# Kernel tuning notes

Hardware: AMD Instinct MI355X
Metric: run time of the kernel (lower is better)

## Reference

```python
import jax, jax.numpy as jnp
import numpy as np

PAD = (1, 1, 1, 1)  # (left, right, top, bottom)
STRIDE = 1

def _blur_kernel(dtype):
    k = jnp.asarray([1.0, 3.0, 3.0, 1.0], dtype=dtype)
    k2 = k[:, None] * k[None, :]
    k2 = k2 / k2.sum()  # normalize=True -> divide by 64
    return k2

def setup_inputs() -> dict:
    key = jax.random.key(0)
    x = jax.random.normal(key, (8, 64, 512, 512), dtype=jnp.float32)
    return {"x": x}

def reference(x):
    B, C, H, W = x.shape
    k2 = _blur_kernel(x.dtype)
    # depthwise kernel: OIHW with O=C, I=1 and feature_group_count=C
    kernel = jnp.broadcast_to(k2[None, None], (C, 1, 4, 4))
    # F.pad order: (left, right, top, bottom) -> pad W then H
    xp = jnp.pad(x, ((0, 0), (0, 0), (PAD[2], PAD[3]), (PAD[0], PAD[1])))
    out = jax.lax.conv_general_dilated(
        xp, kernel,
        window_strides=(STRIDE, STRIDE),
        padding='VALID',
        dimension_numbers=('NCHW', 'OIHW', 'NCHW'),
        feature_group_count=C,
    )
    return out
```

## Files before the change

### kernel.cpp

```cpp
#include <hip/hip_runtime.h>


constexpr int H  = 512;
constexpr int W  = 512;
constexpr int OH = 511;
constexpr int OW = 511;
constexpr int NPLANES = 8 * 64;

typedef float f4u __attribute__((ext_vector_type(4), aligned(4)));

struct Row { float4 A, B, C; };

__device__ __forceinline__ Row ldrow(const float* __restrict__ ip, int gy,
                                     int cb, bool aok, bool cok)
{
    Row r;
    r.A = make_float4(0.f, 0.f, 0.f, 0.f);
    r.B = r.A;
    r.C = r.A;
    if ((unsigned)gy < (unsigned)H) {
        const float* p = ip + (size_t)gy * W + cb;
        r.B = *reinterpret_cast<const float4*>(p);
        if (aok) r.A = *reinterpret_cast<const float4*>(p - 4);
        if (cok) r.C = *reinterpret_cast<const float4*>(p + 4);
    }
    return r;
}

__device__ __forceinline__ float4 hp(const Row& r)
{
    float4 h;
    h.x = (r.A.w + r.B.z) + 3.f * (r.B.x + r.B.y);
    h.y = (r.B.x + r.B.w) + 3.f * (r.B.y + r.B.z);
    h.z = (r.B.y + r.C.x) + 3.f * (r.B.z + r.B.w);
    h.w = (r.B.z + r.C.y) + 3.f * (r.B.w + r.C.x);
    return h;
}

__device__ __forceinline__ float4 vcomb(const float4& h0, const float4& h1,
                                        const float4& h2, const float4& h3)
{
    float4 o;
    o.x = ((h0.x + h3.x) + 3.f * (h1.x + h2.x)) * 0.015625f;
    o.y = ((h0.y + h3.y) + 3.f * (h1.y + h2.y)) * 0.015625f;
    o.z = ((h0.z + h3.z) + 3.f * (h1.z + h2.z)) * 0.015625f;
    o.w = ((h0.w + h3.w) + 3.f * (h1.w + h2.w)) * 0.015625f;
    return o;
}

__device__ __forceinline__ void st(float* __restrict__ op, int oy, int cb,
                                   bool cok, const float4& o)
{
    float* p = op + (size_t)oy * OW + cb;
    if (cok) {
        *reinterpret_cast<f4u*>(p) = (f4u){o.x, o.y, o.z, o.w};
    } else {
        p[0] = o.x; p[1] = o.y; p[2] = o.z;
    }
}

__global__ __launch_bounds__(256)
void blur_kernel(const float* __restrict__ in, float* __restrict__ out)
{
    const int tid   = threadIdx.x;
    const int xt    = tid & 127;
    const int sub   = tid >> 7;
    const int cb    = xt * 4;
    const int plane = blockIdx.x;
    const int ys    = blockIdx.y * 128 + sub * 64;
    const int ye    = min(ys + 64, OH);

    const float* __restrict__ ip = in  + (size_t)plane * (H * W);
    float*       __restrict__ op = out + (size_t)plane * (OH * OW);

    const bool aok = (xt > 0);
    const bool cok = (xt < 127);

    Row r0 = ldrow(ip, ys - 1, cb, aok, cok);
    Row r1 = ldrow(ip, ys,     cb, aok, cok);
    Row r2 = ldrow(ip, ys + 1, cb, aok, cok);
    Row P  = ldrow(ip, ys + 2, cb, aok, cok);
    Row Q  = ldrow(ip, ys + 3, cb, aok, cok);

    float4 h0 = hp(r0);
    float4 h1 = hp(r1);
    float4 h2 = hp(r2);

    int oy = ys;
    while (oy + 1 < ye) {
        float4 h3 = hp(P);
        st(op, oy, cb, cok, vcomb(h0, h1, h2, h3));
        P = ldrow(ip, oy + 4, cb, aok, cok);

        float4 h4 = hp(Q);
        st(op, oy + 1, cb, cok, vcomb(h1, h2, h3, h4));
        Q = ldrow(ip, oy + 5, cb, aok, cok);

        h0 = h2; h1 = h3; h2 = h4;
        oy += 2;
    }
    if (oy < ye) {
        float4 h3 = hp(P);
        st(op, oy, cb, cok, vcomb(h0, h1, h2, h3));
    }
}

extern "C" void kernel_launch(void* const* d_in, const int* in_sizes, int n_in,
                              void* d_out, int out_size, void* d_ws, size_t ws_size,
                              hipStream_t stream)
{
    const float* x = (const float*)d_in[0];
    float* out = (float*)d_out;

    dim3 grid(NPLANES, 4);
    dim3 block(256);
    blur_kernel<<<grid, block, 0, stream>>>(x, out);
}
```

Baseline: 270.4 us.

## Use 8 columns per lane with wavefront shuffles for horizontal halo

Each lane now covers 8 columns, so one 64-lane wavefront spans a full 512-wide row. The horizontal halo comes from neighbouring lanes via shuffles instead of extra overlapping float4 loads. Each wave handles 32 rows with four rows of prefetch in flight, and the last lane's edge column is handled with an overlapping store. This removes redundant global loads and the per-thread halo branches, at the cost of more registers per thread and fewer threads per plane row.

```diff
diff --git a/kernel.cpp b/kernel.cpp
--- a/kernel.cpp
+++ b/kernel.cpp
@@ -9,99 +9,98 @@
 
 typedef float f4u __attribute__((ext_vector_type(4), aligned(4)));
 
-struct Row { float4 A, B, C; };
+struct H8 { float v[8]; };
+struct R2 { float4 b0, b1; };
 
-__device__ __forceinline__ Row ldrow(const float* __restrict__ ip, int gy,
-                                     int cb, bool aok, bool cok)
+__device__ __forceinline__ R2 ldrow(const float* __restrict__ ip, int gy, int cb)
 {
-    Row r;
-    r.A = make_float4(0.f, 0.f, 0.f, 0.f);
-    r.B = r.A;
-    r.C = r.A;
+    R2 r;
+    r.b0 = make_float4(0.f, 0.f, 0.f, 0.f);
+    r.b1 = r.b0;
     if ((unsigned)gy < (unsigned)H) {
         const float* p = ip + (size_t)gy * W + cb;
-        r.B = *reinterpret_cast<const float4*>(p);
-        if (aok) r.A = *reinterpret_cast<const float4*>(p - 4);
-        if (cok) r.C = *reinterpret_cast<const float4*>(p + 4);
+        r.b0 = *reinterpret_cast<const float4*>(p);
+        r.b1 = *reinterpret_cast<const float4*>(p + 4);
     }
     return r;
 }
 
-__device__ __forceinline__ float4 hp(const Row& r)
+__device__ __forceinline__ H8 hp8(const R2& r, bool l0, bool l63)
 {
-    float4 h;
-    h.x = (r.A.w + r.B.z) + 3.f * (r.B.x + r.B.y);
-    h.y = (r.B.x + r.B.w) + 3.f * (r.B.y + r.B.z);
-    h.z = (r.B.y + r.C.x) + 3.f * (r.B.z + r.B.w);
-    h.w = (r.B.z + r.C.y) + 3.f * (r.B.w + r.C.x);
+    float L  = __shfl_up(r.b1.w, 1);
+    float RX = __shfl_down(r.b0.x, 1);
+    float RY = __shfl_down(r.b0.y, 1);
+    L  = l0  ? 0.f : L;
+    RX = l63 ? 0.f : RX;
+    RY = l63 ? 0.f : RY;
+    H8 h;
+    h.v[0] = (L       + r.b0.z) + 3.f * (r.b0.x + r.b0.y);
+    h.v[1] = (r.b0.x  + r.b0.w) + 3.f * (r.b0.y + r.b0.z);
+    h.v[2] = (r.b0.y  + r.b1.x) + 3.f * (r.b0.z + r.b0.w);
+    h.v[3] = (r.b0.z  + r.b1.y) + 3.f * (r.b0.w + r.b1.x);
+    h.v[4] = (r.b0.w  + r.b1.z) + 3.f * (r.b1.x + r.b1.y);
+    h.v[5] = (r.b1.x  + r.b1.w) + 3.f * (r.b1.y + r.b1.z);
+    h.v[6] = (r.b1.y  + RX)     + 3.f * (r.b1.z + r.b1.w);
+    h.v[7] = (r.b1.z  + RY)     + 3.f * (r.b1.w + RX);
     return h;
 }
 
-__device__ __forceinline__ float4 vcomb(const float4& h0, const float4& h1,
-                                        const float4& h2, const float4& h3)
+__device__ __forceinline__ void vst(float* __restrict__ op, int oy, int cb, bool l63,
+                                    const H8& a, const H8& b, const H8& c, const H8& d)
 {
-    float4 o;
-    o.x = ((h0.x + h3.x) + 3.f * (h1.x + h2.x)) * 0.015625f;
-    o.y = ((h0.y + h3.y) + 3.f * (h1.y + h2.y)) * 0.015625f;
-    o.z = ((h0.z + h3.z) + 3.f * (h1.z + h2.z)) * 0.015625f;
-    o.w = ((h0.w + h3.w) + 3.f * (h1.w + h2.w)) * 0.015625f;
-    return o;
-}
-
-__device__ __forceinline__ void st(float* __restrict__ op, int oy, int cb,
-                                   bool cok, const float4& o)
-{
+    if (oy >= OH) return;
+    float o[8];
+    #pragma unroll
+    for (int j = 0; j < 8; ++j)
+        o[j] = ((a.v[j] + d.v[j]) + 3.f * (b.v[j] + c.v[j])) * 0.015625f;
     float* p = op + (size_t)oy * OW + cb;
-    if (cok) {
-        *reinterpret_cast<f4u*>(p) = (f4u){o.x, o.y, o.z, o.w};
-    } else {
-        p[0] = o.x; p[1] = o.y; p[2] = o.z;
-    }
+    *reinterpret_cast<f4u*>(p) = (f4u){o[0], o[1], o[2], o[3]};
+    f4u s2 = { l63 ? o[3] : o[4], l63 ? o[4] : o[5],
+               l63 ? o[5] : o[6], l63 ? o[6] : o[7] };
+    *reinterpret_cast<f4u*>(p + (l63 ? 3 : 4)) = s2;
 }
 
 __global__ __launch_bounds__(256)
 void blur_kernel(const float* __restrict__ in, float* __restrict__ out)
 {
-    const int tid   = threadIdx.x;
-    const int xt    = tid & 127;
-    const int sub   = tid >> 7;
-    const int cb    = xt * 4;
+    const int  tid  = threadIdx.x;
+    const int  lane = tid & 63;
+    const int  wv   = tid >> 6;
+    const bool l0   = (lane == 0), l63 = (lane == 63);
+    const int  cb   = lane * 8;
+
     const int plane = blockIdx.x;
-    const int ys    = blockIdx.y * 128 + sub * 64;
-    const int ye    = min(ys + 64, OH);
+    const int ys    = blockIdx.y * 128 + wv * 32;
 
     const float* __restrict__ ip = in  + (size_t)plane * (H * W);
     float*       __restrict__ op = out + (size_t)plane * (OH * OW);
 
-    const bool aok = (xt > 0);
-    const bool cok = (xt < 127);
+    R2 r0 = ldrow(ip, ys - 1, cb);
+    R2 r1 = ldrow(ip, ys,     cb);
+    R2 r2 = ldrow(ip, ys + 1, cb);
+    R2 P0 = ldrow(ip, ys + 2, cb);
+    R2 P1 = ldrow(ip, ys + 3, cb);
+    R2 P2 = ldrow(ip, ys + 4, cb);
+    R2 P3 = ldrow(ip, ys + 5, cb);
 
-    Row r0 = ldrow(ip, ys - 1, cb, aok, cok);
-    Row r1 = ldrow(ip, ys,     cb, aok, cok);
-    Row r2 = ldrow(ip, ys + 1, cb, aok, cok);
-    Row P  = ldrow(ip, ys + 2, cb, aok, cok);
-    Row Q  = ldrow(ip, ys + 3, cb, aok, cok);
-
-    float4 h0 = hp(r0);
-    float4 h1 = hp(r1);
-    float4 h2 = hp(r2);
+    H8 hA = hp8(r0, l0, l63);
+    H8 hB = hp8(r1, l0, l63);
+    H8 hC = hp8(r2, l0, l63);
 
     int oy = ys;
-    while (oy + 1 < ye) {
-        float4 h3 = hp(P);
-        st(op, oy, cb, cok, vcomb(h0, h1, h2, h3));
-        P = ldrow(ip, oy + 4, cb, aok, cok);
-
-        float4 h4 = hp(Q);
-        st(op, oy + 1, cb, cok, vcomb(h1, h2, h3, h4));
-        Q = ldrow(ip, oy + 5, cb, aok, cok);
-
-        h0 = h2; h1 = h3; h2 = h4;
-        oy += 2;
+    #pragma unroll 1
+    for (; oy < ys + 28; oy += 4) {
+        H8 h3 = hp8(P0, l0, l63); vst(op, oy,     cb, l63, hA, hB, hC, h3); P0 = ldrow(ip, oy + 6, cb);
+        H8 h4 = hp8(P1, l0, l63); vst(op, oy + 1, cb, l63, hB, hC, h3, h4); P1 = ldrow(ip, oy + 7, cb);
+        H8 h5 = hp8(P2, l0, l63); vst(op, oy + 2, cb, l63, hC, h3, h4, h5); P2 = ldrow(ip, oy + 8, cb);
+        H8 h6 = hp8(P3, l0, l63); vst(op, oy + 3, cb, l63, h3, h4, h5, h6); P3 = ldrow(ip, oy + 9, cb);
+        hA = h4; hB = h5; hC = h6;
     }
-    if (oy < ye) {
-        float4 h3 = hp(P);
-        st(op, oy, cb, cok, vcomb(h0, h1, h2, h3));
+    {
+        H8 h3 = hp8(P0, l0, l63); vst(op, oy,     cb, l63, hA, hB, hC, h3);
+        H8 h4 = hp8(P1, l0, l63); vst(op, oy + 1, cb, l63, hB, hC, h3, h4);
+        H8 h5 = hp8(P2, l0, l63); vst(op, oy + 2, cb, l63, hC, h3, h4, h5);
+        H8 h6 = hp8(P3, l0, l63); vst(op, oy + 3, cb, l63, h3, h4, h5, h6);
     }
 }
 
```

Result: faster. 251.6 us (-7.0%).

## Use wave shuffles for horizontal halo and deepen row prefetch pipeline

Applied to the files above, without the earlier changes.

Each thread now loads one float4 per row plus a small float2 halo at the seam between two half-row waves, instead of three float4 loads. Neighbour pixels come from cross-lane shuffles, which cuts redundant global and L1 traffic. The launch becomes one 512-thread block per plane with four row strips of 128, and the rolling pipeline keeps six rows in flight instead of two, for more memory-level parallelism. Stores to the last partial column are realigned with a shuffle so every lane issues one unaligned float4 store, at the cost of extra register pressure and fewer blocks.

```diff
diff --git a/kernel.cpp b/kernel.cpp
--- a/kernel.cpp
+++ b/kernel.cpp
@@ -9,99 +9,119 @@
 
 typedef float f4u __attribute__((ext_vector_type(4), aligned(4)));
 
-struct Row { float4 A, B, C; };
+struct R { float4 q; float2 hx; };
 
-__device__ __forceinline__ Row ldrow(const float* __restrict__ ip, int gy,
-                                     int cb, bool aok, bool cok)
+__device__ __forceinline__ R ldrow(const float* __restrict__ ip, int gy, int side, int lane)
 {
-    Row r;
-    r.A = make_float4(0.f, 0.f, 0.f, 0.f);
-    r.B = r.A;
-    r.C = r.A;
+    R r;
+    r.q  = make_float4(0.f, 0.f, 0.f, 0.f);
+    r.hx = make_float2(0.f, 0.f);
     if ((unsigned)gy < (unsigned)H) {
-        const float* p = ip + (size_t)gy * W + cb;
-        r.B = *reinterpret_cast<const float4*>(p);
-        if (aok) r.A = *reinterpret_cast<const float4*>(p - 4);
-        if (cok) r.C = *reinterpret_cast<const float4*>(p + 4);
+        const float* row = ip + (size_t)gy * W;
+        r.q  = *reinterpret_cast<const float4*>(row + side * 256 + 4 * lane);
+        r.hx = *reinterpret_cast<const float2*>(row + (side ? 254 : 256));
     }
     return r;
 }
 
-__device__ __forceinline__ float4 hp(const Row& r)
+__device__ __forceinline__ float4 hp4(const R& r, int side, bool l0, bool l63)
 {
+    float L  = __shfl_up(r.q.w, 1);
+    float RX = __shfl_down(r.q.x, 1);
+    float RY = __shfl_down(r.q.y, 1);
+    if (side == 0) {
+        if (l0)  L = 0.f;
+        if (l63) { RX = r.hx.x; RY = r.hx.y; }
+    } else {
+        if (l0)  L = r.hx.y;
+        if (l63) { RX = 0.f; RY = 0.f; }
+    }
     float4 h;
-    h.x = (r.A.w + r.B.z) + 3.f * (r.B.x + r.B.y);
-    h.y = (r.B.x + r.B.w) + 3.f * (r.B.y + r.B.z);
-    h.z = (r.B.y + r.C.x) + 3.f * (r.B.z + r.B.w);
-    h.w = (r.B.z + r.C.y) + 3.f * (r.B.w + r.C.x);
+    h.x = (L      + r.q.z) + 3.f * (r.q.x + r.q.y);
+    h.y = (r.q.x  + r.q.w) + 3.f * (r.q.y + r.q.z);
+    h.z = (r.q.y  + RX)    + 3.f * (r.q.z + r.q.w);
+    h.w = (r.q.z  + RY)    + 3.f * (r.q.w + RX);
     return h;
 }
 
-__device__ __forceinline__ float4 vcomb(const float4& h0, const float4& h1,
-                                        const float4& h2, const float4& h3)
+__device__ __forceinline__ void vst(float* __restrict__ op, int oy, int side, int lane,
+                                    bool lastq,
+                                    const float4& a, const float4& b,
+                                    const float4& c, const float4& d)
 {
-    float4 o;
-    o.x = ((h0.x + h3.x) + 3.f * (h1.x + h2.x)) * 0.015625f;
-    o.y = ((h0.y + h3.y) + 3.f * (h1.y + h2.y)) * 0.015625f;
-    o.z = ((h0.z + h3.z) + 3.f * (h1.z + h2.z)) * 0.015625f;
-    o.w = ((h0.w + h3.w) + 3.f * (h1.w + h2.w)) * 0.015625f;
-    return o;
-}
-
-__device__ __forceinline__ void st(float* __restrict__ op, int oy, int cb,
-                                   bool cok, const float4& o)
-{
-    float* p = op + (size_t)oy * OW + cb;
-    if (cok) {
-        *reinterpret_cast<f4u*>(p) = (f4u){o.x, o.y, o.z, o.w};
-    } else {
-        p[0] = o.x; p[1] = o.y; p[2] = o.z;
+    if (oy < OH) {
+        float4 o;
+        o.x = ((a.x + d.x) + 3.f * (b.x + c.x)) * 0.015625f;
+        o.y = ((a.y + d.y) + 3.f * (b.y + c.y)) * 0.015625f;
+        o.z = ((a.z + d.z) + 3.f * (b.z + c.z)) * 0.015625f;
+        o.w = ((a.w + d.w) + 3.f * (b.w + c.w)) * 0.015625f;
+        float ow = __shfl_up(o.w, 1);
+        float* p = op + (size_t)oy * OW + side * 256 + 4 * lane;
+        if (lastq) {
+            f4u s = { ow, o.x, o.y, o.z };
+            *reinterpret_cast<f4u*>(p - 1) = s;
+        } else {
+            f4u s = { o.x, o.y, o.z, o.w };
+            *reinterpret_cast<f4u*>(p) = s;
+        }
     }
 }
 
-__global__ __launch_bounds__(256)
+__global__ __launch_bounds__(512, 4)
 void blur_kernel(const float* __restrict__ in, float* __restrict__ out)
 {
-    const int tid   = threadIdx.x;
-    const int xt    = tid & 127;
-    const int sub   = tid >> 7;
-    const int cb    = xt * 4;
+    const int  tid  = threadIdx.x;
+    const int  lane = tid & 63;
+    const int  wv   = tid >> 6;
+    const int  s    = wv >> 1;
+    const int  side = wv & 1;
+    const bool l0   = (lane == 0), l63 = (lane == 63);
+    const bool lastq = (side == 1) && l63;
+
     const int plane = blockIdx.x;
-    const int ys    = blockIdx.y * 128 + sub * 64;
-    const int ye    = min(ys + 64, OH);
+    const int ys    = s * 128;
 
     const float* __restrict__ ip = in  + (size_t)plane * (H * W);
     float*       __restrict__ op = out + (size_t)plane * (OH * OW);
 
-    const bool aok = (xt > 0);
-    const bool cok = (xt < 127);
+    R r0 = ldrow(ip, ys - 1, side, lane);
+    R r1 = ldrow(ip, ys,     side, lane);
+    R r2 = ldrow(ip, ys + 1, side, lane);
+    R P0 = ldrow(ip, ys + 2, side, lane);
+    R P1 = ldrow(ip, ys + 3, side, lane);
+    R P2 = ldrow(ip, ys + 4, side, lane);
+    R P3 = ldrow(ip, ys + 5, side, lane);
+    R P4 = ldrow(ip, ys + 6, side, lane);
+    R P5 = ldrow(ip, ys + 7, side, lane);
 
-    Row r0 = ldrow(ip, ys - 1, cb, aok, cok);
-    Row r1 = ldrow(ip, ys,     cb, aok, cok);
-    Row r2 = ldrow(ip, ys + 1, cb, aok, cok);
-    Row P  = ldrow(ip, ys + 2, cb, aok, cok);
-    Row Q  = ldrow(ip, ys + 3, cb, aok, cok);
+    float4 hA = hp4(r0, side, l0, l63);
+    float4 hB = hp4(r1, side, l0, l63);
+    float4 hC = hp4(r2, side, l0, l63);
 
-    float4 h0 = hp(r0);
-    float4 h1 = hp(r1);
-    float4 h2 = hp(r2);
+    int i = 0;
+    #pragma unroll 1
+    for (int t = 0; t < 20; ++t, i += 6) {
+        float4 h3;
+        h3 = hp4(P0, side, l0, l63); vst(op, ys + i + 0, side, lane, lastq, hA, hB, hC, h3); P0 = ldrow(ip, ys + i + 8,  side, lane); hA = hB; hB = hC; hC = h3;
+        h3 = hp4(P1, side, l0, l63); vst(op, ys + i + 1, side, lane, lastq, hA, hB, hC, h3); P1 = ldrow(ip, ys + i + 9,  side, lane); hA = hB; hB = hC; hC = h3;
+        h3 = hp4(P2, side, l0, l63); vst(op, ys + i + 2, side, lane, lastq, hA, hB, hC, h3); P2 = ldrow(ip, ys + i + 10, side, lane); hA = hB; hB = hC; hC = h3;
+        h3 = hp4(P3, side, l0, l63); vst(op, ys + i + 3, side, lane, lastq, hA, hB, hC, h3); P3 = ldrow(ip, ys + i + 11, side, lane); hA = hB; hB = hC; hC = h3;
+        h3 = hp4(P4, side, l0, l63); vst(op, ys + i + 4, side, lane, lastq, hA, hB, hC, h3); P4 = ldrow(ip, ys + i + 12, side, lane); hA = hB; hB = hC; hC = h3;
+        h3 = hp4(P5, side, l0, l63); vst(op, ys + i + 5, side, lane, lastq, hA, hB, hC, h3); P5 = ldrow(ip, ys + i + 13, side, lane); hA = hB; hB = hC; hC = h3;
+    }
 
-    int oy = ys;
-    while (oy + 1 < ye) {
-        float4 h3 = hp(P);
-        st(op, oy, cb, cok, vcomb(h0, h1, h2, h3));
-        P = ldrow(ip, oy + 4, cb, aok, cok);
-
-        float4 h4 = hp(Q);
-        st(op, oy + 1, cb, cok, vcomb(h1, h2, h3, h4));
-        Q = ldrow(ip, oy + 5, cb, aok, cok);
-
-        h0 = h2; h1 = h3; h2 = h4;
-        oy += 2;
-    }
-    if (oy < ye) {
-        float4 h3 = hp(P);
-        st(op, oy, cb, cok, vcomb(h0, h1, h2, h3));
+    R Q0 = ldrow(ip, ys + 128, side, lane);
+    R Q1 = ldrow(ip, ys + 129, side, lane);
+    {
+        float4 h3;
+        h3 = hp4(P0, side, l0, l63); vst(op, ys + 120, side, lane, lastq, hA, hB, hC, h3); hA = hB; hB = hC; hC = h3;
+        h3 = hp4(P1, side, l0, l63); vst(op, ys + 121, side, lane, lastq, hA, hB, hC, h3); hA = hB; hB = hC; hC = h3;
+        h3 = hp4(P2, side, l0, l63); vst(op, ys + 122, side, lane, lastq, hA, hB, hC, h3); hA = hB; hB = hC; hC = h3;
+        h3 = hp4(P3, side, l0, l63); vst(op, ys + 123, side, lane, lastq, hA, hB, hC, h3); hA = hB; hB = hC; hC = h3;
+        h3 = hp4(P4, side, l0, l63); vst(op, ys + 124, side, lane, lastq, hA, hB, hC, h3); hA = hB; hB = hC; hC = h3;
+        h3 = hp4(P5, side, l0, l63); vst(op, ys + 125, side, lane, lastq, hA, hB, hC, h3); hA = hB; hB = hC; hC = h3;
+        h3 = hp4(Q0, side, l0, l63); vst(op, ys + 126, side, lane, lastq, hA, hB, hC, h3); hA = hB; hB = hC; hC = h3;
+        h3 = hp4(Q1, side, l0, l63); vst(op, ys + 127, side, lane, lastq, hA, hB, hC, h3);
     }
 }
 
@@ -112,7 +132,7 @@
     const float* x = (const float*)d_in[0];
     float* out = (float*)d_out;
 
-    dim3 grid(NPLANES, 4);
-    dim3 block(256);
+    dim3 grid(NPLANES);
+    dim3 block(512);
     blur_kernel<<<grid, block, 0, stream>>>(x, out);
 }
```

Result: faster. 245.0 us (-9.4%).
